# Optimization experiments

Measured on AMD Instinct MI355X. Metric: run time of the kernel, lower is better.

The kernel has to match this reference:

```python
import jax, jax.numpy as jnp
import numpy as np

NUM_EXPERTS = 8
TOP_K = 2

def setup_inputs() -> dict:
    key = jax.random.key(0)
    ks = jax.random.split(key, 5)
    B, S, H, I, E = 4, 2048, 1024, 2816, NUM_EXPERTS
    return {
        "hidden_states": jax.random.normal(ks[0], (B, S, H), dtype=jnp.float32),
        "gate_w": jax.random.normal(ks[1], (H, E), dtype=jnp.float32) / np.sqrt(H),
        "w_gate": jax.random.normal(ks[2], (E, H, I), dtype=jnp.float32) / np.sqrt(H),
        "w_up": jax.random.normal(ks[3], (E, H, I), dtype=jnp.float32) / np.sqrt(H),
        "w_down": jax.random.normal(ks[4], (E, I, H), dtype=jnp.float32) / np.sqrt(I),
    }

def reference(hidden_states, gate_w, w_gate, w_up, w_down):
    B, S, H = hidden_states.shape
    x = hidden_states.reshape(-1, H)                      # [T, H]
    router_logits = x @ gate_w                            # [T, E]
    probs = jax.nn.softmax(router_logits.astype(jnp.float32), axis=-1)
    topk_w, sel = jax.lax.top_k(probs, TOP_K)             # [T, K]
    topk_w = topk_w / jnp.sum(topk_w, axis=-1, keepdims=True)
    topk_w = topk_w.astype(x.dtype)
    out = jnp.zeros_like(x)
    for e in range(NUM_EXPERTS):
        # combine weight for this expert per token (0 if not routed)
        we = jnp.sum(jnp.where(sel == e, topk_w, 0.0), axis=-1)  # [T]
        h = jax.nn.silu(x @ w_gate[e]) * (x @ w_up[e])           # [T, I]
        out = out + (h @ w_down[e]) * we[:, None]
    return out.reshape(B, S, H), router_logits
```

## Files before the change

kernel.cpp:

```cpp
#include <hip/hip_runtime.h>
#include <hip/hip_bf16.h>
#include <stdint.h>

typedef unsigned short u16;
typedef unsigned int u32;

#define T_TOK 8192
#define H_DIM 1024
#define I_DIM 2816
#define NE 8

typedef __bf16 bf16x8 __attribute__((ext_vector_type(8)));
typedef float f32x4 __attribute__((ext_vector_type(4)));

union F8 { uint4 v; bf16x8 f; u32 w[4]; };

__device__ __forceinline__ u16 f2bf(float f) {
    u32 u = __float_as_uint(f);
    u32 r = u + 0x7FFFu + ((u >> 16) & 1u);
    return (u16)(r >> 16);
}
__device__ __forceinline__ u32 pkbf(float a, float b) {
    float2 f; f.x = a; f.y = b;
    __hip_bfloat162 h = __float22bfloat162_rn(f);
    union { __hip_bfloat162 h2; u32 w; } cv; cv.h2 = h;
    return cv.w;
}

__device__ __forceinline__ void g2l16(const void* g, void* l) {
    __builtin_amdgcn_global_load_lds(
        (const __attribute__((address_space(1))) u32*)g,
        (__attribute__((address_space(3))) u32*)l, 16, 0, 0);
}

__global__ void zero_cnt_kernel(int* __restrict__ cnt) {
    if (threadIdx.x < NE) cnt[threadIdx.x] = 0;
}

__global__ void __launch_bounds__(256) zero_out_kernel(float* __restrict__ out0) {
    int gid = blockIdx.x * 256 + threadIdx.x;
    f32x4 z = {0.f, 0.f, 0.f, 0.f};
    ((f32x4*)out0)[gid] = z;
}

__global__ void __launch_bounds__(256) xcvt_kernel(const float* __restrict__ x, u16* __restrict__ xb) {
    size_t gid = (size_t)blockIdx.x * 256 + threadIdx.x;
    const float4* s = (const float4*)x + gid * 2;
    float4 a = s[0], b = s[1];
    uint4 o;
    o.x = pkbf(a.x, a.y); o.y = pkbf(a.z, a.w);
    o.z = pkbf(b.x, b.y); o.w = pkbf(b.z, b.w);
    ((uint4*)xb)[gid] = o;
}

__global__ void __launch_bounds__(256)
pack_kernel(const float* __restrict__ src, u32* __restrict__ dst, int K, int N) {
    int e = blockIdx.z;
    int n0 = blockIdx.x * 64;
    int r0 = blockIdx.y * 128;
    __shared__ float sT[128][65];
    int tid = threadIdx.x;
    const float* sp = src + ((size_t)e * K + r0) * N + n0;
#pragma unroll
    for (int rep = 0; rep < 8; rep++) {
        int row = rep * 16 + (tid >> 4);
        int n4 = (tid & 15) * 4;
        float4 v = *(const float4*)(sp + (size_t)row * N + n4);
        sT[row][n4] = v.x; sT[row][n4 + 1] = v.y; sT[row][n4 + 2] = v.z; sT[row][n4 + 3] = v.w;
    }
    __syncthreads();
    int n = tid >> 2, q = tid & 3;
    u32* dp = dst + ((size_t)e * N + n0 + n) * (size_t)(K >> 1) + (r0 >> 1) + q * 16;
    uint4 o[4];
    u32* ow = (u32*)o;
#pragma unroll
    for (int j = 0; j < 16; j++) {
        int k2 = q * 16 + j;
        ow[j] = pkbf(sT[2 * k2][n], sT[2 * k2 + 1][n]);
    }
#pragma unroll
    for (int j = 0; j < 4; j++) ((uint4*)dp)[j] = o[j];
}

__global__ void __launch_bounds__(256)
router_kernel(const float* __restrict__ x, const float* __restrict__ gw,
              float* __restrict__ logits_out, float* __restrict__ wbuf,
              int* __restrict__ cnt, int* __restrict__ idxlist) {
    int lane = threadIdx.x & 63;
    int t = blockIdx.x * 4 + (threadIdx.x >> 6);
    const float* xr = x + (size_t)t * H_DIM;
    float acc[NE];
#pragma unroll
    for (int e = 0; e < NE; e++) acc[e] = 0.f;
#pragma unroll
    for (int i = 0; i < 16; i++) {
        int hh = i * 64 + lane;
        float xv = xr[hh];
        const float4* grow = (const float4*)(gw + (size_t)hh * NE);
        float4 g0 = grow[0], g1 = grow[1];
        acc[0] += xv * g0.x; acc[1] += xv * g0.y;
        acc[2] += xv * g0.z; acc[3] += xv * g0.w;
        acc[4] += xv * g1.x; acc[5] += xv * g1.y;
        acc[6] += xv * g1.z; acc[7] += xv * g1.w;
    }
#pragma unroll
    for (int m = 32; m >= 1; m >>= 1) {
#pragma unroll
        for (int e = 0; e < NE; e++) acc[e] += __shfl_xor(acc[e], m, 64);
    }
    if (lane == 0) {
        float mx = acc[0];
#pragma unroll
        for (int e = 1; e < NE; e++) mx = fmaxf(mx, acc[e]);
        float p[NE];
#pragma unroll
        for (int e = 0; e < NE; e++) p[e] = __expf(acc[e] - mx);
        float4 l0, l1;
        l0.x = acc[0]; l0.y = acc[1]; l0.z = acc[2]; l0.w = acc[3];
        l1.x = acc[4]; l1.y = acc[5]; l1.z = acc[6]; l1.w = acc[7];
        float4* lrow_p = (float4*)(logits_out + (size_t)t * NE);
        lrow_p[0] = l0; lrow_p[1] = l1;
        int a = 0; float pa = p[0];
#pragma unroll
        for (int e = 1; e < NE; e++) if (p[e] > pa) { a = e; pa = p[e]; }
        int b = -1; float pb = -1.f;
#pragma unroll
        for (int e = 0; e < NE; e++) if (e != a && p[e] > pb) { b = e; pb = p[e]; }
        if (b < 0) { b = a ^ 1; pb = p[b]; }
        float inv = 1.f / (pa + pb);
        wbuf[2 * t]     = pa * inv;
        wbuf[2 * t + 1] = pb * inv;
        int pos = atomicAdd(&cnt[a], 1); idxlist[a * T_TOK + pos] = 2 * t;
        pos = atomicAdd(&cnt[b], 1);     idxlist[b * T_TOK + pos] = 2 * t + 1;
    }
}

__global__ void __launch_bounds__(512, 2)
gateup_kernel(const u16* __restrict__ xb, const u32* __restrict__ wgp,
              const u32* __restrict__ wup, const int* __restrict__ cnt,
              const int* __restrict__ idxlist, u16* __restrict__ hchunk,
              int nbase, int nlen) {
    int NN = nlen >> 7;
    int pid = blockIdx.x;
    int xcd = pid & 7;
    int j = pid >> 3;
    int m = j & 31;
    int gs = j >> 5;
    int g = xcd + (gs << 3);
    int e = g / NN;
    int nb = g - e * NN;
    int c = cnt[e];
    int m0 = m * 256;
    if (m0 >= c) return;
    int n0l = nb * 128;
    int n0g = nbase + n0l;

    __shared__ alignas(16) u16 sA[2][256 * 64];
    __shared__ alignas(16) u32 sBg[2][128 * 32];
    __shared__ alignas(16) u32 sBu[2][128 * 32];
    int tid = threadIdx.x;
    int wv = tid >> 6;

    int arow = tid >> 3;
    int csw = tid & 7;
    const u16* aP[4];
#pragma unroll
    for (int p = 0; p < 4; p++) {
        int jj = m0 + p * 64 + arow; if (jj > c - 1) jj = c - 1;
        int slot = idxlist[e * T_TOK + jj];
        aP[p] = xb + (size_t)(slot >> 1) * H_DIM + ((csw ^ (arow & 7)) << 3);
    }
    size_t bn = (size_t)e * I_DIM + n0g + arow;
    int bsw = (csw ^ (arow & 7)) << 2;
    const u32* bgB = wgp + bn * 512 + bsw;
    const u32* buB = wup + bn * 512 + bsw;

    auto stage = [&](int k0, int buf) {
#pragma unroll
        for (int p = 0; p < 4; p++)
            g2l16(aP[p] + k0, &sA[buf][(p * 64 + wv * 8) * 64]);
#pragma unroll
        for (int p2 = 0; p2 < 2; p2++)
            g2l16(bgB + (size_t)p2 * 64 * 512 + (k0 >> 1), &sBg[buf][(p2 * 64 + wv * 8) * 32]);
#pragma unroll
        for (int p2 = 0; p2 < 2; p2++)
            g2l16(buB + (size_t)p2 * 64 * 512 + (k0 >> 1), &sBu[buf][(p2 * 64 + wv * 8) * 32]);
    };

    int lane = tid & 63;
    int wm = wv >> 1, wn = wv & 1;
    int lrow = lane & 15, quad = lane >> 4;
    f32x4 zero = {0.f, 0.f, 0.f, 0.f};
    f32x4 accg[4][4], accu[4][4];
#pragma unroll
    for (int mi = 0; mi < 4; mi++)
#pragma unroll
        for (int ni = 0; ni < 4; ni++) { accg[mi][ni] = zero; accu[mi][ni] = zero; }

    stage(0, 0);
#pragma unroll 2
    for (int k0 = 0; k0 < H_DIM; k0 += 64) {
        int buf = (k0 >> 6) & 1;
        __syncthreads();
        if (k0 + 64 < H_DIM) stage(k0 + 64, buf ^ 1);
#pragma unroll
        for (int kk = 0; kk < 2; kk++) {
            int cb = kk * 4 + quad;
            bf16x8 af[4]; F8 bg[4], bu[4];
#pragma unroll
            for (int i = 0; i < 4; i++) {
                int ra = wm * 64 + i * 16 + lrow;
                af[i] = *(const bf16x8*)&sA[buf][(size_t)(ra * 8 + (cb ^ (ra & 7))) * 8];
                int n = wn * 64 + i * 16 + lrow;
                bg[i].v = *(const uint4*)&sBg[buf][(size_t)(n * 8 + (cb ^ (n & 7))) * 4];
                bu[i].v = *(const uint4*)&sBu[buf][(size_t)(n * 8 + (cb ^ (n & 7))) * 4];
            }
#pragma unroll
            for (int mi = 0; mi < 4; mi++)
#pragma unroll
                for (int ni = 0; ni < 4; ni++) {
                    accg[mi][ni] = __builtin_amdgcn_mfma_f32_16x16x32_bf16(af[mi], bg[ni].f, accg[mi][ni], 0, 0, 0);
                    accu[mi][ni] = __builtin_amdgcn_mfma_f32_16x16x32_bf16(af[mi], bu[ni].f, accu[mi][ni], 0, 0, 0);
                }
        }
    }

    u16* hT = &sA[0][0];
    __syncthreads();
#pragma unroll
    for (int mi = 0; mi < 4; mi++) {
#pragma unroll
        for (int r = 0; r < 4; r++) {
            int row = wm * 64 + mi * 16 + quad * 4 + r;
            int swz = (row & 7) << 3;
#pragma unroll
            for (int ni = 0; ni < 4; ni++) {
                int col = wn * 64 + ni * 16 + lrow;
                float gv = accg[mi][ni][r], uv = accu[mi][ni][r];
                float hv = gv * uv / (1.f + __expf(-gv));
                hT[row * 128 + (col ^ swz)] = f2bf(hv);
            }
        }
    }
    __syncthreads();
    {
        int row = tid >> 1, half = tid & 1;
        int grow = m0 + row;
        if (grow < c) {
            int slot = idxlist[e * T_TOK + grow];
            u16* dst = hchunk + (size_t)slot * nlen + n0l + half * 64;
            int swz = (row & 7) << 3;
#pragma unroll
            for (int j2 = 0; j2 < 8; j2++) {
                int colb = half * 64 + j2 * 8;
                *(uint4*)(dst + j2 * 8) = *(const uint4*)&hT[row * 128 + (colb ^ swz)];
            }
        }
    }
}

__global__ void __launch_bounds__(512, 2)
down_kernel(const u16* __restrict__ hchunk, const u32* __restrict__ wdp,
            const int* __restrict__ cnt, const int* __restrict__ idxlist,
            const float* __restrict__ wbuf, float* __restrict__ out0,
            float* __restrict__ ybuf, int kbase, int klen, int beta) {
    int pid = blockIdx.x;
    int xcd = pid & 7;
    int j = pid >> 3;
    int m = j & 31;
    int gs = j >> 5;
    int g = xcd + (gs << 3);
    int e = g >> 3;
    int nb = g & 7;
    int c = cnt[e];
    int m0 = m * 256;
    if (m0 >= c) return;
    int n0 = nb * 128;

    __shared__ alignas(16) u16 sA[2][256 * 64];
    __shared__ alignas(16) u32 sB[2][128 * 32];
    int tid = threadIdx.x;
    int wv = tid >> 6;

    int arow = tid >> 3;
    int csw = tid & 7;
    const u16* aP[4];
#pragma unroll
    for (int p = 0; p < 4; p++) {
        int jj = m0 + p * 64 + arow; if (jj > c - 1) jj = c - 1;
        int slot = idxlist[e * T_TOK + jj];
        aP[p] = hchunk + (size_t)slot * klen + ((csw ^ (arow & 7)) << 3);
    }
    int bsw = (csw ^ (arow & 7)) << 2;
    const u32* bB = wdp + ((size_t)e * H_DIM + n0 + arow) * 1408 + (kbase >> 1) + bsw;

    auto stage = [&](int k0, int buf) {
#pragma unroll
        for (int p = 0; p < 4; p++)
            g2l16(aP[p] + k0, &sA[buf][(p * 64 + wv * 8) * 64]);
#pragma unroll
        for (int p2 = 0; p2 < 2; p2++)
            g2l16(bB + (size_t)p2 * 64 * 1408 + (k0 >> 1), &sB[buf][(p2 * 64 + wv * 8) * 32]);
    };

    int lane = tid & 63;
    int wm = wv >> 1, wn = wv & 1;
    int lrow = lane & 15, quad = lane >> 4;
    f32x4 zero = {0.f, 0.f, 0.f, 0.f};
    f32x4 acc[4][4];
#pragma unroll
    for (int mi = 0; mi < 4; mi++)
#pragma unroll
        for (int ni = 0; ni < 4; ni++) acc[mi][ni] = zero;

    stage(0, 0);
#pragma unroll 2
    for (int k0 = 0; k0 < klen; k0 += 64) {
        int buf = (k0 >> 6) & 1;
        __syncthreads();
        if (k0 + 64 < klen) stage(k0 + 64, buf ^ 1);
#pragma unroll
        for (int kk = 0; kk < 2; kk++) {
            int cb = kk * 4 + quad;
            bf16x8 af[4]; F8 bf[4];
#pragma unroll
            for (int i = 0; i < 4; i++) {
                int ra = wm * 64 + i * 16 + lrow;
                af[i] = *(const bf16x8*)&sA[buf][(size_t)(ra * 8 + (cb ^ (ra & 7))) * 8];
                int n = wn * 64 + i * 16 + lrow;
                bf[i].v = *(const uint4*)&sB[buf][(size_t)(n * 8 + (cb ^ (n & 7))) * 4];
            }
#pragma unroll
            for (int mi = 0; mi < 4; mi++)
#pragma unroll
                for (int ni = 0; ni < 4; ni++)
                    acc[mi][ni] = __builtin_amdgcn_mfma_f32_16x16x32_bf16(af[mi], bf[ni].f, acc[mi][ni], 0, 0, 0);
        }
    }
#pragma unroll
    for (int mi = 0; mi < 4; mi++) {
#pragma unroll
        for (int r = 0; r < 4; r++) {
            int grow = m0 + wm * 64 + mi * 16 + quad * 4 + r;
            if (grow < c) {
                int slot = idxlist[e * T_TOK + grow];
                if (ybuf) {
                    float* yrow = ybuf + (size_t)slot * H_DIM + n0 + wn * 64 + lrow;
                    if (beta) {
#pragma unroll
                        for (int ni = 0; ni < 4; ni++) yrow[ni * 16] += acc[mi][ni][r];
                    } else {
#pragma unroll
                        for (int ni = 0; ni < 4; ni++) yrow[ni * 16] = acc[mi][ni][r];
                    }
                } else {
                    float w = wbuf[slot];
                    float* yrow = out0 + (size_t)(slot >> 1) * H_DIM + n0 + wn * 64 + lrow;
#pragma unroll
                    for (int ni = 0; ni < 4; ni++)
                        atomicAdd(&yrow[ni * 16], w * acc[mi][ni][r]);
                }
            }
        }
    }
}

__global__ void __launch_bounds__(256)
combine_kernel(const float* __restrict__ ybuf, const float* __restrict__ wbuf,
               float* __restrict__ out0) {
    int gid = blockIdx.x * 256 + threadIdx.x;
    int t = gid >> 8;
    int h4 = gid & 255;
    float w0 = wbuf[2 * t], w1 = wbuf[2 * t + 1];
    f32x4 a = ((const f32x4*)(ybuf + (size_t)(2 * t) * H_DIM))[h4];
    f32x4 b = ((const f32x4*)(ybuf + (size_t)(2 * t + 1) * H_DIM))[h4];
    f32x4 o;
#pragma unroll
    for (int i = 0; i < 4; i++) o[i] = w0 * a[i] + w1 * b[i];
    ((f32x4*)(out0 + (size_t)t * H_DIM))[h4] = o;
}

extern "C" void kernel_launch(void* const* d_in, const int* in_sizes, int n_in,
                              void* d_out, int out_size, void* d_ws, size_t ws_size,
                              hipStream_t stream) {
    (void)in_sizes; (void)n_in; (void)out_size;
    const float* x  = (const float*)d_in[0];
    const float* gw = (const float*)d_in[1];
    const float* wg = (const float*)d_in[2];
    const float* wu = (const float*)d_in[3];
    const float* wd = (const float*)d_in[4];
    float* out = (float*)d_out;
    float* logits = out + (size_t)T_TOK * H_DIM;
    char* ws = (char*)d_ws;

    size_t off = 0;
    auto take = [&](size_t sz) { char* p = ws + off; off += (sz + 255) & ~(size_t)255; return p; };
    int* cnt      = (int*)take(NE * 4);
    int* idxlist  = (int*)take((size_t)NE * T_TOK * 4);
    float* wbuf   = (float*)take((size_t)2 * T_TOK * 4);
    u16* xb       = (u16*)take((size_t)T_TOK * H_DIM * 2);
    u32* wgp      = (u32*)take((size_t)NE * I_DIM * 512 * 4);
    u32* wup      = (u32*)take((size_t)NE * I_DIM * 512 * 4);
    u32* wdp      = (u32*)take((size_t)NE * H_DIM * 1408 * 4);
    float* ybuf = nullptr;
    size_t ybytes = (size_t)2 * T_TOK * H_DIM * 4;
    size_t minh   = (size_t)2 * T_TOK * 128 * 2 + 256;
    if (ws_size >= off + ybytes + minh) ybuf = (float*)take(ybytes);
    int ich = I_DIM;
    while (ich > 128 && off + (size_t)2 * T_TOK * ich * 2 > ws_size) ich -= 128;
    u16* hchunk = (u16*)(ws + off);

    zero_cnt_kernel<<<1, 64, 0, stream>>>(cnt);
    if (!ybuf) zero_out_kernel<<<T_TOK * H_DIM / 4 / 256, 256, 0, stream>>>(out);
    pack_kernel<<<dim3(I_DIM / 64, H_DIM / 128, NE), 256, 0, stream>>>(wg, wgp, H_DIM, I_DIM);
    pack_kernel<<<dim3(I_DIM / 64, H_DIM / 128, NE), 256, 0, stream>>>(wu, wup, H_DIM, I_DIM);
    pack_kernel<<<dim3(H_DIM / 64, I_DIM / 128, NE), 256, 0, stream>>>(wd, wdp, I_DIM, H_DIM);
    xcvt_kernel<<<T_TOK * H_DIM / 8 / 256, 256, 0, stream>>>(x, xb);
    router_kernel<<<T_TOK / 4, 256, 0, stream>>>(x, gw, logits, wbuf, cnt, idxlist);
    for (int base = 0; base < I_DIM; base += ich) {
        int len = I_DIM - base; if (len > ich) len = ich;
        int NN = len / 128;
        gateup_kernel<<<8 * 32 * NN, 512, 0, stream>>>(xb, wgp, wup, cnt, idxlist, hchunk, base, len);
        down_kernel<<<8 * 32 * 8, 512, 0, stream>>>(hchunk, wdp, cnt, idxlist, wbuf, out, ybuf, base, len, base > 0 ? 1 : 0);
    }
    if (ybuf) combine_kernel<<<T_TOK * H_DIM / 4 / 256, 256, 0, stream>>>(ybuf, wbuf, out);
}
```

Before: 1.196 ms.

## Interleave gate/up weights and use 256x256 tiles with split-phase pipelined MFMA loops

Packs gate and up weights row-interleaved into one buffer, so one B tile of 256 columns covers 128 gate/up pairs. The SiLU product is then formed by exchanging neighbouring lanes with a shuffle. Both GEMM kernels move to 256x256 output tiles at one block per CU, with manual vmcnt waits, split A staging across two MFMA halves, and s_setprio around the MFMA bursts. The aim is more reuse per loaded tile and better overlap of global-to-LDS loads with compute, at the cost of higher register pressure and lower occupancy.

New measurement: 1.093 ms. 1.09x faster.

```diff
diff --git a/kernel.cpp b/kernel.cpp
--- a/kernel.cpp
+++ b/kernel.cpp
@@ -32,6 +32,9 @@
         (const __attribute__((address_space(1))) u32*)g,
         (__attribute__((address_space(3))) u32*)l, 16, 0, 0);
 }
+
+#define VM_BAR(n) asm volatile("s_waitcnt vmcnt(" #n ")\ns_barrier" ::: "memory")
+#define VM_WAIT(n) asm volatile("s_waitcnt vmcnt(" #n ")" ::: "memory")
 
 __global__ void zero_cnt_kernel(int* __restrict__ cnt) {
     if (threadIdx.x < NE) cnt[threadIdx.x] = 0;
@@ -54,7 +57,8 @@
 }
 
 __global__ void __launch_bounds__(256)
-pack_kernel(const float* __restrict__ src, u32* __restrict__ dst, int K, int N) {
+pack_kernel(const float* __restrict__ src, u32* __restrict__ dst, int K, int N,
+            int rmul, int radd) {
     int e = blockIdx.z;
     int n0 = blockIdx.x * 64;
     int r0 = blockIdx.y * 128;
@@ -70,7 +74,8 @@
     }
     __syncthreads();
     int n = tid >> 2, q = tid & 3;
-    u32* dp = dst + ((size_t)e * N + n0 + n) * (size_t)(K >> 1) + (r0 >> 1) + q * 16;
+    u32* dp = dst + ((size_t)e * N * rmul + (size_t)rmul * (n0 + n) + radd) * (size_t)(K >> 1)
+                  + (r0 >> 1) + q * 16;
     uint4 o[4];
     u32* ow = (u32*)o;
 #pragma unroll
@@ -135,18 +140,19 @@
     }
 }
 
-__global__ void __launch_bounds__(512, 2)
-gateup_kernel(const u16* __restrict__ xb, const u32* __restrict__ wgp,
-              const u32* __restrict__ wup, const int* __restrict__ cnt,
-              const int* __restrict__ idxlist, u16* __restrict__ hchunk,
-              int nbase, int nlen) {
+__global__ void __launch_bounds__(512, 1)
+gateup_kernel(const u16* __restrict__ xb, const u32* __restrict__ wb,
+              const int* __restrict__ cnt, const int* __restrict__ idxlist,
+              u16* __restrict__ hchunk, int nbase, int nlen) {
     int NN = nlen >> 7;
+    int ngrp = NE * NN;
     int pid = blockIdx.x;
     int xcd = pid & 7;
     int j = pid >> 3;
     int m = j & 31;
     int gs = j >> 5;
     int g = xcd + (gs << 3);
+    if (g >= ngrp) return;
     int e = g / NN;
     int nb = g - e * NN;
     int c = cnt[e];
@@ -156,89 +162,126 @@
     int n0g = nbase + n0l;
 
     __shared__ alignas(16) u16 sA[2][256 * 64];
-    __shared__ alignas(16) u32 sBg[2][128 * 32];
-    __shared__ alignas(16) u32 sBu[2][128 * 32];
+    __shared__ alignas(16) u32 sB[2][256 * 32];
     int tid = threadIdx.x;
     int wv = tid >> 6;
 
-    int arow = tid >> 3;
-    int csw = tid & 7;
+    int r = tid >> 3;
+    int ch = tid & 7;
+    int sw8 = (ch ^ (r & 7)) << 3;
+    int sw4 = (ch ^ (r & 7)) << 2;
     const u16* aP[4];
 #pragma unroll
-    for (int p = 0; p < 4; p++) {
-        int jj = m0 + p * 64 + arow; if (jj > c - 1) jj = c - 1;
+    for (int q = 0; q < 4; q++) {
+        int jj = m0 + q * 64 + r; if (jj > c - 1) jj = c - 1;
         int slot = idxlist[e * T_TOK + jj];
-        aP[p] = xb + (size_t)(slot >> 1) * H_DIM + ((csw ^ (arow & 7)) << 3);
-    }
-    size_t bn = (size_t)e * I_DIM + n0g + arow;
-    int bsw = (csw ^ (arow & 7)) << 2;
-    const u32* bgB = wgp + bn * 512 + bsw;
-    const u32* buB = wup + bn * 512 + bsw;
-
-    auto stage = [&](int k0, int buf) {
-#pragma unroll
-        for (int p = 0; p < 4; p++)
-            g2l16(aP[p] + k0, &sA[buf][(p * 64 + wv * 8) * 64]);
-#pragma unroll
-        for (int p2 = 0; p2 < 2; p2++)
-            g2l16(bgB + (size_t)p2 * 64 * 512 + (k0 >> 1), &sBg[buf][(p2 * 64 + wv * 8) * 32]);
-#pragma unroll
-        for (int p2 = 0; p2 < 2; p2++)
-            g2l16(buB + (size_t)p2 * 64 * 512 + (k0 >> 1), &sBu[buf][(p2 * 64 + wv * 8) * 32]);
+        aP[q] = xb + (size_t)(slot >> 1) * H_DIM + sw8;
+    }
+    size_t b0 = ((size_t)e * I_DIM + n0g) * 2;
+    const u32* bP[4];
+#pragma unroll
+    for (int q = 0; q < 4; q++) bP[q] = wb + (b0 + q * 64 + r) * 512 + sw4;
+
+    auto stageB4 = [&](int k0, int b) {
+#pragma unroll
+        for (int q = 0; q < 4; q++)
+            g2l16(bP[q] + (k0 >> 1), &sB[b][q * 2048 + wv * 256]);
     };
+    auto stageA4 = [&](int k0, int b) {
+        g2l16(aP[0] + k0, &sA[b][0 * 4096 + wv * 512]);
+        g2l16(aP[2] + k0, &sA[b][2 * 4096 + wv * 512]);
+        g2l16(aP[1] + k0, &sA[b][1 * 4096 + wv * 512]);
+        g2l16(aP[3] + k0, &sA[b][3 * 4096 + wv * 512]);
+    };
 
     int lane = tid & 63;
-    int wm = wv >> 1, wn = wv & 1;
+    int wm = wv >> 2, wn = wv & 3;
     int lrow = lane & 15, quad = lane >> 4;
     f32x4 zero = {0.f, 0.f, 0.f, 0.f};
-    f32x4 accg[4][4], accu[4][4];
-#pragma unroll
-    for (int mi = 0; mi < 4; mi++)
-#pragma unroll
-        for (int ni = 0; ni < 4; ni++) { accg[mi][ni] = zero; accu[mi][ni] = zero; }
-
-    stage(0, 0);
-#pragma unroll 2
-    for (int k0 = 0; k0 < H_DIM; k0 += 64) {
-        int buf = (k0 >> 6) & 1;
-        __syncthreads();
-        if (k0 + 64 < H_DIM) stage(k0 + 64, buf ^ 1);
-#pragma unroll
-        for (int kk = 0; kk < 2; kk++) {
-            int cb = kk * 4 + quad;
-            bf16x8 af[4]; F8 bg[4], bu[4];
-#pragma unroll
-            for (int i = 0; i < 4; i++) {
-                int ra = wm * 64 + i * 16 + lrow;
-                af[i] = *(const bf16x8*)&sA[buf][(size_t)(ra * 8 + (cb ^ (ra & 7))) * 8];
-                int n = wn * 64 + i * 16 + lrow;
-                bg[i].v = *(const uint4*)&sBg[buf][(size_t)(n * 8 + (cb ^ (n & 7))) * 4];
-                bu[i].v = *(const uint4*)&sBu[buf][(size_t)(n * 8 + (cb ^ (n & 7))) * 4];
+    f32x4 acc[8][4];
+#pragma unroll
+    for (int mi = 0; mi < 8; mi++)
+#pragma unroll
+        for (int nr = 0; nr < 4; nr++) acc[mi][nr] = zero;
+
+    stageB4(0, 0);
+    stageA4(0, 0);
+    for (int t = 0; t < 16; t++) {
+        int cb_ = t & 1;
+        VM_BAR(2);
+        if (t < 15) stageB4((t + 1) * 64, cb_ ^ 1);
+        F8 bfr[4][2];
+#pragma unroll
+        for (int nr = 0; nr < 4; nr++)
+#pragma unroll
+            for (int kk = 0; kk < 2; kk++) {
+                int n = wn * 64 + nr * 16 + lrow;
+                int ph = (kk * 4 + quad) ^ (n & 7);
+                bfr[nr][kk].v = *(const uint4*)&sB[cb_][(n * 8 + ph) * 4];
             }
-#pragma unroll
-            for (int mi = 0; mi < 4; mi++)
-#pragma unroll
-                for (int ni = 0; ni < 4; ni++) {
-                    accg[mi][ni] = __builtin_amdgcn_mfma_f32_16x16x32_bf16(af[mi], bg[ni].f, accg[mi][ni], 0, 0, 0);
-                    accu[mi][ni] = __builtin_amdgcn_mfma_f32_16x16x32_bf16(af[mi], bu[ni].f, accu[mi][ni], 0, 0, 0);
+        {
+            bf16x8 af[4][2];
+#pragma unroll
+            for (int mi = 0; mi < 4; mi++)
+#pragma unroll
+                for (int kk = 0; kk < 2; kk++) {
+                    int R = wm * 128 + mi * 16 + lrow;
+                    int ph = (kk * 4 + quad) ^ (R & 7);
+                    af[mi][kk] = *(const bf16x8*)&sA[cb_][(R * 8 + ph) * 8];
                 }
+            __builtin_amdgcn_s_setprio(1);
+#pragma unroll
+            for (int mi = 0; mi < 4; mi++)
+#pragma unroll
+                for (int nr = 0; nr < 4; nr++)
+#pragma unroll
+                    for (int kk = 0; kk < 2; kk++)
+                        acc[mi][nr] = __builtin_amdgcn_mfma_f32_16x16x32_bf16(af[mi][kk], bfr[nr][kk].f, acc[mi][nr], 0, 0, 0);
+            __builtin_amdgcn_s_setprio(0);
+        }
+        if (t < 15) { stageA4((t + 1) * 64, cb_ ^ 1); VM_WAIT(8); }
+        else        { VM_WAIT(0); }
+        {
+            bf16x8 af[4][2];
+#pragma unroll
+            for (int mi = 0; mi < 4; mi++)
+#pragma unroll
+                for (int kk = 0; kk < 2; kk++) {
+                    int R = wm * 128 + 64 + mi * 16 + lrow;
+                    int ph = (kk * 4 + quad) ^ (R & 7);
+                    af[mi][kk] = *(const bf16x8*)&sA[cb_][(R * 8 + ph) * 8];
+                }
+            __builtin_amdgcn_s_setprio(1);
+#pragma unroll
+            for (int mi = 0; mi < 4; mi++)
+#pragma unroll
+                for (int nr = 0; nr < 4; nr++)
+#pragma unroll
+                    for (int kk = 0; kk < 2; kk++)
+                        acc[mi + 4][nr] = __builtin_amdgcn_mfma_f32_16x16x32_bf16(af[mi][kk], bfr[nr][kk].f, acc[mi + 4][nr], 0, 0, 0);
+            __builtin_amdgcn_s_setprio(0);
         }
     }
 
     u16* hT = &sA[0][0];
     __syncthreads();
 #pragma unroll
-    for (int mi = 0; mi < 4; mi++) {
-#pragma unroll
-        for (int r = 0; r < 4; r++) {
-            int row = wm * 64 + mi * 16 + quad * 4 + r;
+    for (int mi = 0; mi < 8; mi++) {
+#pragma unroll
+        for (int rr = 0; rr < 4; rr++) {
+            int row = wm * 128 + mi * 16 + quad * 4 + rr;
             int swz = (row & 7) << 3;
 #pragma unroll
-            for (int ni = 0; ni < 4; ni++) {
-                int col = wn * 64 + ni * 16 + lrow;
-                float gv = accg[mi][ni][r], uv = accu[mi][ni][r];
+            for (int nr = 0; nr < 4; nr++) {
+                float mine = acc[mi][nr][rr];
+                float other = __shfl_xor(mine, 1, 64);
+                float gv = (lane & 1) ? other : mine;
+                float uv = (lane & 1) ? mine : other;
                 float hv = gv * uv / (1.f + __expf(-gv));
-                hT[row * 128 + (col ^ swz)] = f2bf(hv);
+                if (!(lane & 1)) {
+                    int colp = wn * 32 + nr * 8 + (lrow >> 1);
+                    hT[row * 128 + (colp ^ swz)] = f2bf(hv);
+                }
             }
         }
     }
@@ -259,7 +302,7 @@
     }
 }
 
-__global__ void __launch_bounds__(512, 2)
+__global__ void __launch_bounds__(512, 1)
 down_kernel(const u16* __restrict__ hchunk, const u32* __restrict__ wdp,
             const int* __restrict__ cnt, const int* __restrict__ idxlist,
             const float* __restrict__ wbuf, float* __restrict__ out0,
@@ -270,95 +313,137 @@
     int m = j & 31;
     int gs = j >> 5;
     int g = xcd + (gs << 3);
-    int e = g >> 3;
-    int nb = g & 7;
+    int e = g >> 2;
+    int nb = g & 3;
     int c = cnt[e];
     int m0 = m * 256;
     if (m0 >= c) return;
-    int n0 = nb * 128;
+    int n0 = nb * 256;
 
     __shared__ alignas(16) u16 sA[2][256 * 64];
-    __shared__ alignas(16) u32 sB[2][128 * 32];
+    __shared__ alignas(16) u32 sB[2][256 * 32];
     int tid = threadIdx.x;
     int wv = tid >> 6;
 
-    int arow = tid >> 3;
-    int csw = tid & 7;
+    int r = tid >> 3;
+    int ch = tid & 7;
+    int sw8 = (ch ^ (r & 7)) << 3;
+    int sw4 = (ch ^ (r & 7)) << 2;
     const u16* aP[4];
 #pragma unroll
-    for (int p = 0; p < 4; p++) {
-        int jj = m0 + p * 64 + arow; if (jj > c - 1) jj = c - 1;
+    for (int q = 0; q < 4; q++) {
+        int jj = m0 + q * 64 + r; if (jj > c - 1) jj = c - 1;
         int slot = idxlist[e * T_TOK + jj];
-        aP[p] = hchunk + (size_t)slot * klen + ((csw ^ (arow & 7)) << 3);
-    }
-    int bsw = (csw ^ (arow & 7)) << 2;
-    const u32* bB = wdp + ((size_t)e * H_DIM + n0 + arow) * 1408 + (kbase >> 1) + bsw;
-
-    auto stage = [&](int k0, int buf) {
-#pragma unroll
-        for (int p = 0; p < 4; p++)
-            g2l16(aP[p] + k0, &sA[buf][(p * 64 + wv * 8) * 64]);
-#pragma unroll
-        for (int p2 = 0; p2 < 2; p2++)
-            g2l16(bB + (size_t)p2 * 64 * 1408 + (k0 >> 1), &sB[buf][(p2 * 64 + wv * 8) * 32]);
+        aP[q] = hchunk + (size_t)slot * klen + sw8;
+    }
+    const u32* bP[4];
+#pragma unroll
+    for (int q = 0; q < 4; q++)
+        bP[q] = wdp + ((size_t)e * H_DIM + n0 + q * 64 + r) * 1408 + (kbase >> 1) + sw4;
+
+    auto stageB4 = [&](int k0, int b) {
+#pragma unroll
+        for (int q = 0; q < 4; q++)
+            g2l16(bP[q] + (k0 >> 1), &sB[b][q * 2048 + wv * 256]);
     };
+    auto stageA4 = [&](int k0, int b) {
+        g2l16(aP[0] + k0, &sA[b][0 * 4096 + wv * 512]);
+        g2l16(aP[2] + k0, &sA[b][2 * 4096 + wv * 512]);
+        g2l16(aP[1] + k0, &sA[b][1 * 4096 + wv * 512]);
+        g2l16(aP[3] + k0, &sA[b][3 * 4096 + wv * 512]);
+    };
 
     int lane = tid & 63;
-    int wm = wv >> 1, wn = wv & 1;
+    int wm = wv >> 2, wn = wv & 3;
     int lrow = lane & 15, quad = lane >> 4;
     f32x4 zero = {0.f, 0.f, 0.f, 0.f};
-    f32x4 acc[4][4];
-#pragma unroll
-    for (int mi = 0; mi < 4; mi++)
-#pragma unroll
-        for (int ni = 0; ni < 4; ni++) acc[mi][ni] = zero;
-
-    stage(0, 0);
-#pragma unroll 2
-    for (int k0 = 0; k0 < klen; k0 += 64) {
-        int buf = (k0 >> 6) & 1;
-        __syncthreads();
-        if (k0 + 64 < klen) stage(k0 + 64, buf ^ 1);
-#pragma unroll
-        for (int kk = 0; kk < 2; kk++) {
-            int cb = kk * 4 + quad;
-            bf16x8 af[4]; F8 bf[4];
-#pragma unroll
-            for (int i = 0; i < 4; i++) {
-                int ra = wm * 64 + i * 16 + lrow;
-                af[i] = *(const bf16x8*)&sA[buf][(size_t)(ra * 8 + (cb ^ (ra & 7))) * 8];
-                int n = wn * 64 + i * 16 + lrow;
-                bf[i].v = *(const uint4*)&sB[buf][(size_t)(n * 8 + (cb ^ (n & 7))) * 4];
+    f32x4 acc[8][4];
+#pragma unroll
+    for (int mi = 0; mi < 8; mi++)
+#pragma unroll
+        for (int nr = 0; nr < 4; nr++) acc[mi][nr] = zero;
+
+    int NT = klen >> 6;
+    stageB4(0, 0);
+    stageA4(0, 0);
+    for (int t = 0; t < NT; t++) {
+        int cb_ = t & 1;
+        VM_BAR(2);
+        if (t < NT - 1) stageB4((t + 1) * 64, cb_ ^ 1);
+        F8 bfr[4][2];
+#pragma unroll
+        for (int nr = 0; nr < 4; nr++)
+#pragma unroll
+            for (int kk = 0; kk < 2; kk++) {
+                int n = wn * 64 + nr * 16 + lrow;
+                int ph = (kk * 4 + quad) ^ (n & 7);
+                bfr[nr][kk].v = *(const uint4*)&sB[cb_][(n * 8 + ph) * 4];
             }
-#pragma unroll
-            for (int mi = 0; mi < 4; mi++)
-#pragma unroll
-                for (int ni = 0; ni < 4; ni++)
-                    acc[mi][ni] = __builtin_amdgcn_mfma_f32_16x16x32_bf16(af[mi], bf[ni].f, acc[mi][ni], 0, 0, 0);
-        }
-    }
-#pragma unroll
-    for (int mi = 0; mi < 4; mi++) {
-#pragma unroll
-        for (int r = 0; r < 4; r++) {
-            int grow = m0 + wm * 64 + mi * 16 + quad * 4 + r;
+        {
+            bf16x8 af[4][2];
+#pragma unroll
+            for (int mi = 0; mi < 4; mi++)
+#pragma unroll
+                for (int kk = 0; kk < 2; kk++) {
+                    int R = wm * 128 + mi * 16 + lrow;
+                    int ph = (kk * 4 + quad) ^ (R & 7);
+                    af[mi][kk] = *(const bf16x8*)&sA[cb_][(R * 8 + ph) * 8];
+                }
+            __builtin_amdgcn_s_setprio(1);
+#pragma unroll
+            for (int mi = 0; mi < 4; mi++)
+#pragma unroll
+                for (int nr = 0; nr < 4; nr++)
+#pragma unroll
+                    for (int kk = 0; kk < 2; kk++)
+                        acc[mi][nr] = __builtin_amdgcn_mfma_f32_16x16x32_bf16(af[mi][kk], bfr[nr][kk].f, acc[mi][nr], 0, 0, 0);
+            __builtin_amdgcn_s_setprio(0);
+        }
+        if (t < NT - 1) { stageA4((t + 1) * 64, cb_ ^ 1); VM_WAIT(8); }
+        else            { VM_WAIT(0); }
+        {
+            bf16x8 af[4][2];
+#pragma unroll
+            for (int mi = 0; mi < 4; mi++)
+#pragma unroll
+                for (int kk = 0; kk < 2; kk++) {
+                    int R = wm * 128 + 64 + mi * 16 + lrow;
+                    int ph = (kk * 4 + quad) ^ (R & 7);
+                    af[mi][kk] = *(const bf16x8*)&sA[cb_][(R * 8 + ph) * 8];
+                }
+            __builtin_amdgcn_s_setprio(1);
+#pragma unroll
+            for (int mi = 0; mi < 4; mi++)
+#pragma unroll
+                for (int nr = 0; nr < 4; nr++)
+#pragma unroll
+                    for (int kk = 0; kk < 2; kk++)
+                        acc[mi + 4][nr] = __builtin_amdgcn_mfma_f32_16x16x32_bf16(af[mi][kk], bfr[nr][kk].f, acc[mi + 4][nr], 0, 0, 0);
+            __builtin_amdgcn_s_setprio(0);
+        }
+    }
+#pragma unroll
+    for (int mi = 0; mi < 8; mi++) {
+#pragma unroll
+        for (int rr = 0; rr < 4; rr++) {
+            int grow = m0 + wm * 128 + mi * 16 + quad * 4 + rr;
             if (grow < c) {
                 int slot = idxlist[e * T_TOK + grow];
                 if (ybuf) {
                     float* yrow = ybuf + (size_t)slot * H_DIM + n0 + wn * 64 + lrow;
                     if (beta) {
 #pragma unroll
-                        for (int ni = 0; ni < 4; ni++) yrow[ni * 16] += acc[mi][ni][r];
+                        for (int nr = 0; nr < 4; nr++) yrow[nr * 16] += acc[mi][nr][rr];
                     } else {
 #pragma unroll
-                        for (int ni = 0; ni < 4; ni++) yrow[ni * 16] = acc[mi][ni][r];
+                        for (int nr = 0; nr < 4; nr++) yrow[nr * 16] = acc[mi][nr][rr];
                     }
                 } else {
                     float w = wbuf[slot];
                     float* yrow = out0 + (size_t)(slot >> 1) * H_DIM + n0 + wn * 64 + lrow;
 #pragma unroll
-                    for (int ni = 0; ni < 4; ni++)
-                        atomicAdd(&yrow[ni * 16], w * acc[mi][ni][r]);
+                    for (int nr = 0; nr < 4; nr++)
+                        atomicAdd(&yrow[nr * 16], w * acc[mi][nr][rr]);
                 }
             }
         }
@@ -399,8 +484,7 @@
     int* idxlist  = (int*)take((size_t)NE * T_TOK * 4);
     float* wbuf   = (float*)take((size_t)2 * T_TOK * 4);
     u16* xb       = (u16*)take((size_t)T_TOK * H_DIM * 2);
-    u32* wgp      = (u32*)take((size_t)NE * I_DIM * 512 * 4);
-    u32* wup      = (u32*)take((size_t)NE * I_DIM * 512 * 4);
+    u32* wb       = (u32*)take((size_t)NE * I_DIM * 2 * 512 * 4);
     u32* wdp      = (u32*)take((size_t)NE * H_DIM * 1408 * 4);
     float* ybuf = nullptr;
     size_t ybytes = (size_t)2 * T_TOK * H_DIM * 4;
@@ -412,16 +496,18 @@
 
     zero_cnt_kernel<<<1, 64, 0, stream>>>(cnt);
     if (!ybuf) zero_out_kernel<<<T_TOK * H_DIM / 4 / 256, 256, 0, stream>>>(out);
-    pack_kernel<<<dim3(I_DIM / 64, H_DIM / 128, NE), 256, 0, stream>>>(wg, wgp, H_DIM, I_DIM);
-    pack_kernel<<<dim3(I_DIM / 64, H_DIM / 128, NE), 256, 0, stream>>>(wu, wup, H_DIM, I_DIM);
-    pack_kernel<<<dim3(H_DIM / 64, I_DIM / 128, NE), 256, 0, stream>>>(wd, wdp, I_DIM, H_DIM);
+    pack_kernel<<<dim3(I_DIM / 64, H_DIM / 128, NE), 256, 0, stream>>>(wg, wb, H_DIM, I_DIM, 2, 0);
+    pack_kernel<<<dim3(I_DIM / 64, H_DIM / 128, NE), 256, 0, stream>>>(wu, wb, H_DIM, I_DIM, 2, 1);
+    pack_kernel<<<dim3(H_DIM / 64, I_DIM / 128, NE), 256, 0, stream>>>(wd, wdp, I_DIM, H_DIM, 1, 0);
     xcvt_kernel<<<T_TOK * H_DIM / 8 / 256, 256, 0, stream>>>(x, xb);
     router_kernel<<<T_TOK / 4, 256, 0, stream>>>(x, gw, logits, wbuf, cnt, idxlist);
     for (int base = 0; base < I_DIM; base += ich) {
         int len = I_DIM - base; if (len > ich) len = ich;
         int NN = len / 128;
-        gateup_kernel<<<8 * 32 * NN, 512, 0, stream>>>(xb, wgp, wup, cnt, idxlist, hchunk, base, len);
-        down_kernel<<<8 * 32 * 8, 512, 0, stream>>>(hchunk, wdp, cnt, idxlist, wbuf, out, ybuf, base, len, base > 0 ? 1 : 0);
+        int ngrp = NE * NN;
+        int gcnt = (ngrp + 7) / 8;
+        gateup_kernel<<<8 * 32 * gcnt, 512, 0, stream>>>(xb, wb, cnt, idxlist, hchunk, base, len);
+        down_kernel<<<8 * 32 * 4, 512, 0, stream>>>(hchunk, wdp, cnt, idxlist, wbuf, out, ybuf, base, len, base > 0 ? 1 : 0);
     }
     if (ybuf) combine_kernel<<<T_TOK * H_DIM / 4 / 256, 256, 0, stream>>>(ybuf, wbuf, out);
 }
```
